# Kernel optimization log

Hardware: AMD Instinct MI355X
Metric: run time of the kernel (lower is better)

Reference implementation:

```python
import jax, jax.numpy as jnp
import numpy as np

B, D, E = 8192, 4096, 64
TOP_K = 2
NOISE_EPSILON = 0.01


def setup_inputs() -> dict:
    key = jax.random.key(0)
    k1, k2, k3, k4 = jax.random.split(key, 4)
    return {
        "x": jax.random.normal(k1, (B, D), dtype=jnp.float32),
        # nn.Linear weights, init std=0.1, no bias; torch stores [out, in]
        "gate_w": jax.random.normal(k2, (E, D), dtype=jnp.float32) * 0.1,
        "noise_gate_w": jax.random.normal(k3, (E, D), dtype=jnp.float32) * 0.1,
        # deterministic stand-in for torch.randn_like(clean_logits)
        "noise": jax.random.normal(k4, (B, E), dtype=jnp.float32),
    }


def reference(x, gate_w, noise_gate_w, noise):
    # clean_logits = x @ W_g^T : [B, E]
    clean_logits = jnp.einsum("bd,ed->be", x, gate_w)
    # training path: noisy logits with softplus-scaled noise
    noise_logits = jnp.einsum("bd,ed->be", x, noise_gate_w)
    noisy_logits = clean_logits + noise * jax.nn.softplus(noise_logits) * NOISE_EPSILON
    # top-k over experts, softmax over the k selected logits
    top_k_logits, top_k_indices = jax.lax.top_k(noisy_logits, TOP_K)  # [B, k]
    top_k_gates = jax.nn.softmax(top_k_logits, axis=-1)
    # scatter back into dense [B, E] gates
    rows = jnp.arange(noisy_logits.shape[0])[:, None]  # [B, 1]
    gates = jnp.zeros_like(noisy_logits).at[rows, top_k_indices].set(top_k_gates)
    load = jax.nn.softmax(clean_logits, axis=-1)
    return (gates, load)
```

## Files before the change

### kernel.cpp

```cpp
#include <hip/hip_runtime.h>
#include <math.h>

#define BB 8192
#define DD 4096
#define EE 64

constexpr float NOISE_EPS = 0.01f;
constexpr int BM  = 64;
constexpr int BK  = 32;

typedef __attribute__((ext_vector_type(8))) _Float16 f16x8;
typedef __attribute__((ext_vector_type(4))) float    f32x4;

__device__ __forceinline__ void split8(const float4& a, const float4& b,
                                       f16x8& hi, f16x8& mi) {
    float v[8] = {a.x, a.y, a.z, a.w, b.x, b.y, b.z, b.w};
    #pragma unroll
    for (int j = 0; j < 8; ++j) {
        _Float16 h = (_Float16)v[j];
        hi[j] = h;
        mi[j] = (_Float16)(v[j] - (float)h);
    }
}

__device__ __forceinline__ void gl_lds16(const void* g, void* l) {
    __builtin_amdgcn_global_load_lds(
        (const __attribute__((address_space(1))) unsigned*)g,
        (__attribute__((address_space(3))) unsigned*)l, 16, 0, 0);
}

__global__ __launch_bounds__(256) void wsplit_pack(
    const float* __restrict__ gw, const float* __restrict__ ngw,
    char* __restrict__ wpk)
{
    const int gid = blockIdx.x * 256 + threadIdx.x;
    const int r   = gid >> 9;
    const int kc  = gid & 511;
    const int k0  = kc * 8;
    const float* src = (r < EE) ? gw + (size_t)r * DD + k0
                                : ngw + (size_t)(r - EE) * DD + k0;
    float4 a = *reinterpret_cast<const float4*>(src);
    float4 b = *reinterpret_cast<const float4*>(src + 4);
    f16x8 hi, mi;
    split8(a, b, hi, mi);
    const int T    = k0 >> 5;
    const int kq   = (k0 >> 3) & 3;
    const int cb   = r >> 4;
    const int lane = kq * 16 + (r & 15);
    char* base = wpk + (size_t)T * 16384;
    *reinterpret_cast<f16x8*>(base + ((cb * 2 + 0) * 64 + lane) * 16) = hi;
    *reinterpret_cast<f16x8*>(base + ((cb * 2 + 1) * 64 + lane) * 16) = mi;
}

template <int SK>
__global__ __launch_bounds__(512, 4) void gating_main(
    const float* __restrict__ x,
    const char*  __restrict__ wpk,
    float* __restrict__ partial)
{
    constexpr int KC  = DD / SK;
    constexpr int NKS = KC / BK;

    __shared__ __align__(1024) char xbuf[3][8192];
    __shared__ __align__(1024) char wbuf[2][16384];

    const int tid  = threadIdx.x;
    const int bid  = blockIdx.x;
    const int sk   = bid & (SK - 1);
    const int row0 = (bid / SK) * BM;
    const int lane = tid & 63;
    const int wv   = tid >> 6;
    const int wmi  = wv >> 1;
    const int wni  = wv & 1;
    const int l15  = lane & 15;
    const int kq   = lane >> 4;

    const int xrow = tid >> 3;
    const int xch  = tid & 7;
    const float* xg = x + (size_t)(row0 + xrow) * DD + sk * KC
                        + ((xch ^ (xrow & 7)) << 2);
    const char* wg = wpk + (size_t)(sk * NKS) * 16384 + tid * 16;

    const int ldst = wv * 1024;

    const int ar = wmi * 16 + l15;
    const int xoff0 = ar * 128 + (((kq * 2 + 0) ^ (ar & 7)) << 4);
    const int xoff1 = ar * 128 + (((kq * 2 + 1) ^ (ar & 7)) << 4);
    int boff[4][2];
    #pragma unroll
    for (int nb = 0; nb < 4; ++nb) {
        const int cb = wni * 4 + nb;
        boff[nb][0] = ((cb * 2 + 0) * 64 + lane) * 16;
        boff[nb][1] = ((cb * 2 + 1) * 64 + lane) * 16;
    }

    f32x4 acc[4];
    #pragma unroll
    for (int nb = 0; nb < 4; ++nb) acc[nb] = {0.f, 0.f, 0.f, 0.f};

    char* xc  = (char*)xbuf[0];
    char* xn1 = (char*)xbuf[1];
    char* xn2 = (char*)xbuf[2];
    char* wc  = (char*)wbuf[0];
    char* wn  = (char*)wbuf[1];

    gl_lds16(wg,                wc + ldst);
    gl_lds16(wg + 8192,         wc + 8192 + ldst);
    gl_lds16(xg,                xc + ldst);
    gl_lds16(wg + 16384,        wn + ldst);
    gl_lds16(wg + 16384 + 8192, wn + 8192 + ldst);
    gl_lds16(xg + BK,           xn1 + ldst);
    gl_lds16(xg + 2 * BK,       xn2 + ldst);
    asm volatile("s_waitcnt vmcnt(4)" ::: "memory");
    __builtin_amdgcn_s_barrier();

    for (int t = 0; t < NKS; ++t) {
        f16x8 ah, am;
        {
            float4 a0 = *reinterpret_cast<const float4*>(xc + xoff0);
            float4 a1 = *reinterpret_cast<const float4*>(xc + xoff1);
            split8(a0, a1, ah, am);
        }
        #pragma unroll
        for (int nb = 0; nb < 4; ++nb) {
            f16x8 bh = *reinterpret_cast<const f16x8*>(wc + boff[nb][0]);
            f16x8 bm = *reinterpret_cast<const f16x8*>(wc + boff[nb][1]);
            acc[nb] = __builtin_amdgcn_mfma_f32_16x16x32_f16(ah, bh, acc[nb], 0, 0, 0);
            acc[nb] = __builtin_amdgcn_mfma_f32_16x16x32_f16(am, bh, acc[nb], 0, 0, 0);
            acc[nb] = __builtin_amdgcn_mfma_f32_16x16x32_f16(ah, bm, acc[nb], 0, 0, 0);
        }

        asm volatile("s_waitcnt lgkmcnt(0)" ::: "memory");
        __builtin_amdgcn_s_barrier();

        const int tw = (t + 2 < NKS) ? (t + 2) : (NKS - 1);
        const int tx = (t + 3 < NKS) ? (t + 3) : (NKS - 1);
        gl_lds16(wg + (size_t)tw * 16384,        wc + ldst);
        gl_lds16(wg + (size_t)tw * 16384 + 8192, wc + 8192 + ldst);
        gl_lds16(xg + (size_t)tx * BK,           xc + ldst);
        asm volatile("s_waitcnt vmcnt(4)" ::: "memory");
        __builtin_amdgcn_s_barrier();

        char* xt = xc; xc = xn1; xn1 = xn2; xn2 = xt;
        char* wt = wc; wc = wn;  wn  = wt;
    }
    asm volatile("s_waitcnt vmcnt(0)" ::: "memory");

    const size_t pbase = ((size_t)sk * BB + row0) * 128;
    #pragma unroll
    for (int nb = 0; nb < 4; ++nb) {
        #pragma unroll
        for (int j = 0; j < 4; ++j) {
            const int r = wmi * 16 + kq * 4 + j;
            const int c = wni * 64 + nb * 16 + l15;
            partial[pbase + (size_t)r * 128 + c] = acc[nb][j];
        }
    }
}

template <int SK>
__global__ __launch_bounds__(512) void gating_epi(
    const float* __restrict__ partial,
    const float* __restrict__ noise,
    float* __restrict__ out)
{
    const int tid  = threadIdx.x;
    const int wv   = tid >> 6;
    const int lane = tid & 63;
    const int l15  = lane & 15;
    const int kq   = lane >> 4;
    const int grow = blockIdx.x * 32 + wv * 4 + kq;
    const int s    = l15;

    const float* pb = partial + (size_t)grow * 128 + 4 * s;
    float4 c4 = {0.f,0.f,0.f,0.f}, n4 = {0.f,0.f,0.f,0.f};
    #pragma unroll
    for (int k = 0; k < SK; ++k) {
        const float* p = pb + (size_t)k * BB * 128;
        float4 a = *reinterpret_cast<const float4*>(p);
        float4 b = *reinterpret_cast<const float4*>(p + 64);
        c4.x += a.x; c4.y += a.y; c4.z += a.z; c4.w += a.w;
        n4.x += b.x; n4.y += b.y; n4.z += b.z; n4.w += b.w;
    }

    float4 nz = *reinterpret_cast<const float4*>(noise + (size_t)grow * EE + 4 * s);

    float cc[4] = {c4.x, c4.y, c4.z, c4.w};
    float nl[4] = {n4.x, n4.y, n4.z, n4.w};
    float m1 = -3.4e38f, m2 = -3.4e38f;
    int   i1 = -1, i2 = -1;
    float cmax = -3.4e38f;
    #pragma unroll
    for (int j = 0; j < 4; ++j) {
        const int e = 4 * s + j;
        float sp  = fmaxf(nl[j], 0.0f) + log1pf(expf(-fabsf(nl[j])));
        float nzj = (j == 0) ? nz.x : (j == 1) ? nz.y : (j == 2) ? nz.z : nz.w;
        float vno = fmaf(nzj * sp, NOISE_EPS, cc[j]);
        if (vno > m1)      { m2 = m1; i2 = i1; m1 = vno; i1 = e; }
        else if (vno > m2) { m2 = vno; i2 = e; }
        cmax = fmaxf(cmax, cc[j]);
    }

    #pragma unroll
    for (int m = 1; m < 16; m <<= 1) {
        float b1 = __shfl_xor(m1, m, 16);
        int  bi1 = __shfl_xor(i1, m, 16);
        float b2 = __shfl_xor(m2, m, 16);
        int  bi2 = __shfl_xor(i2, m, 16);
        cmax = fmaxf(cmax, __shfl_xor(cmax, m, 16));

        bool bwin = (b1 > m1) || (b1 == m1 && bi1 < i1);
        float t1; int ti1; float t2; int ti2;
        if (bwin) {
            t1 = b1; ti1 = bi1;
            bool aw = (m1 > b2) || (m1 == b2 && i1 < bi2);
            t2 = aw ? m1 : b2; ti2 = aw ? i1 : bi2;
        } else {
            t1 = m1; ti1 = i1;
            bool bw = (b1 > m2) || (b1 == m2 && bi1 < i2);
            t2 = bw ? b1 : m2; ti2 = bw ? bi1 : i2;
        }
        m1 = t1; i1 = ti1; m2 = t2; i2 = ti2;
    }

    float tq = expf(m2 - m1);
    float p1 = 1.0f / (1.0f + tq);
    float p2 = tq * p1;

    float e0 = expf(cc[0] - cmax);
    float e1 = expf(cc[1] - cmax);
    float e2 = expf(cc[2] - cmax);
    float e3 = expf(cc[3] - cmax);
    float sum = e0 + e1 + e2 + e3;
    #pragma unroll
    for (int m = 1; m < 16; m <<= 1) sum += __shfl_xor(sum, m, 16);
    float inv = 1.0f / sum;

    const int eb = 4 * s;
    float4 gt;
    gt.x = (eb     == i1) ? p1 : (eb     == i2) ? p2 : 0.0f;
    gt.y = (eb + 1 == i1) ? p1 : (eb + 1 == i2) ? p2 : 0.0f;
    gt.z = (eb + 2 == i1) ? p1 : (eb + 2 == i2) ? p2 : 0.0f;
    gt.w = (eb + 3 == i1) ? p1 : (eb + 3 == i2) ? p2 : 0.0f;
    float4 ld = {e0 * inv, e1 * inv, e2 * inv, e3 * inv};

    *reinterpret_cast<float4*>(out + (size_t)grow * EE + eb) = gt;
    *reinterpret_cast<float4*>(out + (size_t)BB * EE + (size_t)grow * EE + eb) = ld;
}

extern "C" void kernel_launch(void* const* d_in, const int* in_sizes, int n_in,
                              void* d_out, int out_size, void* d_ws, size_t ws_size,
                              hipStream_t stream) {
    const float* x     = (const float*)d_in[0];
    const float* gw    = (const float*)d_in[1];
    const float* ngw   = (const float*)d_in[2];
    const float* noise = (const float*)d_in[3];
    float* out = (float*)d_out;

    char*  wpk     = (char*)d_ws;
    float* partial = (float*)(wpk + (size_t)2 * 1024 * 1024);

    const size_t MB = 1024 * 1024;

    hipLaunchKernelGGL(wsplit_pack, dim3(256), dim3(256), 0, stream, gw, ngw, wpk);

    if (ws_size >= 18 * MB) {
        hipLaunchKernelGGL(gating_main<4>, dim3((BB / BM) * 4), dim3(512), 0, stream,
                           x, wpk, partial);
        hipLaunchKernelGGL(gating_epi<4>, dim3(BB / 32), dim3(512), 0, stream,
                           partial, noise, out);
    } else if (ws_size >= 10 * MB) {
        hipLaunchKernelGGL(gating_main<2>, dim3((BB / BM) * 2), dim3(512), 0, stream,
                           x, wpk, partial);
        hipLaunchKernelGGL(gating_epi<2>, dim3(BB / 32), dim3(512), 0, stream,
                           partial, noise, out);
    } else {
        hipLaunchKernelGGL(gating_main<1>, dim3(BB / BM), dim3(512), 0, stream,
                           x, wpk, partial);
        hipLaunchKernelGGL(gating_epi<1>, dim3(BB / 32), dim3(512), 0, stream,
                           partial, noise, out);
    }
}
```

Before: 52.17 us.

## Load packed weights directly to registers and retile waves as 2x4 grid

The weight tiles are no longer staged through LDS. Each wave loads its B fragments straight from global memory into registers, double-buffered one k-step ahead. Waves are rearranged into a 2x4 grid so each wave covers 32 rows and 32 columns, reusing its A fragments across two column blocks. The x ring grows to four buffers, and the loop is unrolled by two with a single barrier per step. This removes LDS traffic and a barrier for the weights but leans on L2 to serve duplicated weight loads, and it uses more registers.

```diff
diff --git a/kernel.cpp b/kernel.cpp
--- a/kernel.cpp
+++ b/kernel.cpp
@@ -61,8 +61,7 @@
     constexpr int KC  = DD / SK;
     constexpr int NKS = KC / BK;
 
-    __shared__ __align__(1024) char xbuf[3][8192];
-    __shared__ __align__(1024) char wbuf[2][16384];
+    __shared__ __align__(1024) char xbuf[4][8192];
 
     const int tid  = threadIdx.x;
     const int bid  = blockIdx.x;
@@ -70,8 +69,8 @@
     const int row0 = (bid / SK) * BM;
     const int lane = tid & 63;
     const int wv   = tid >> 6;
-    const int wmi  = wv >> 1;
-    const int wni  = wv & 1;
+    const int m2   = wv & 1;
+    const int n2   = wv >> 1;
     const int l15  = lane & 15;
     const int kq   = lane >> 4;
 
@@ -79,82 +78,102 @@
     const int xch  = tid & 7;
     const float* xg = x + (size_t)(row0 + xrow) * DD + sk * KC
                         + ((xch ^ (xrow & 7)) << 2);
-    const char* wg = wpk + (size_t)(sk * NKS) * 16384 + tid * 16;
-
     const int ldst = wv * 1024;
-
-    const int ar = wmi * 16 + l15;
-    const int xoff0 = ar * 128 + (((kq * 2 + 0) ^ (ar & 7)) << 4);
-    const int xoff1 = ar * 128 + (((kq * 2 + 1) ^ (ar & 7)) << 4);
-    int boff[4][2];
-    #pragma unroll
-    for (int nb = 0; nb < 4; ++nb) {
-        const int cb = wni * 4 + nb;
-        boff[nb][0] = ((cb * 2 + 0) * 64 + lane) * 16;
-        boff[nb][1] = ((cb * 2 + 1) * 64 + lane) * 16;
-    }
-
-    f32x4 acc[4];
-    #pragma unroll
-    for (int nb = 0; nb < 4; ++nb) acc[nb] = {0.f, 0.f, 0.f, 0.f};
-
-    char* xc  = (char*)xbuf[0];
-    char* xn1 = (char*)xbuf[1];
-    char* xn2 = (char*)xbuf[2];
-    char* wc  = (char*)wbuf[0];
-    char* wn  = (char*)wbuf[1];
-
-    gl_lds16(wg,                wc + ldst);
-    gl_lds16(wg + 8192,         wc + 8192 + ldst);
-    gl_lds16(xg,                xc + ldst);
-    gl_lds16(wg + 16384,        wn + ldst);
-    gl_lds16(wg + 16384 + 8192, wn + 8192 + ldst);
-    gl_lds16(xg + BK,           xn1 + ldst);
-    gl_lds16(xg + 2 * BK,       xn2 + ldst);
-    asm volatile("s_waitcnt vmcnt(4)" ::: "memory");
+    char* xls = (char*)&xbuf[0][0];
+
+    int xoff[2][2];
+    #pragma unroll
+    for (int mb = 0; mb < 2; ++mb) {
+        const int ar = m2 * 32 + mb * 16 + l15;
+        #pragma unroll
+        for (int u = 0; u < 2; ++u)
+            xoff[mb][u] = ar * 128 + (((kq * 2 + u) ^ (ar & 7)) << 4);
+    }
+
+    const char* wgB = wpk + ((size_t)(sk * NKS) << 14) + lane * 16;
+    const int off_h0 = ((n2 * 2 + 0) * 2 + 0) * 1024;
+    const int off_m0 = ((n2 * 2 + 0) * 2 + 1) * 1024;
+    const int off_h1 = ((n2 * 2 + 1) * 2 + 0) * 1024;
+    const int off_m1 = ((n2 * 2 + 1) * 2 + 1) * 1024;
+
+    f32x4 acc00 = {0.f,0.f,0.f,0.f}, acc01 = {0.f,0.f,0.f,0.f};
+    f32x4 acc10 = {0.f,0.f,0.f,0.f}, acc11 = {0.f,0.f,0.f,0.f};
+
+    #define LOADB(t, BH0, BM0, BH1, BM1) do {                                  \
+        const char* _b = wgB + ((size_t)(t) << 14);                            \
+        BH0 = *reinterpret_cast<const f16x8*>(_b + off_h0);                    \
+        BM0 = *reinterpret_cast<const f16x8*>(_b + off_m0);                    \
+        BH1 = *reinterpret_cast<const f16x8*>(_b + off_h1);                    \
+        BM1 = *reinterpret_cast<const f16x8*>(_b + off_m1);                    \
+    } while (0)
+
+    #define COMPUTE(t, BH0, BM0, BH1, BM1) do {                                \
+        const char* _xb = xls + (((t) & 3) << 13);                             \
+        float4 a00 = *reinterpret_cast<const float4*>(_xb + xoff[0][0]);       \
+        float4 a01 = *reinterpret_cast<const float4*>(_xb + xoff[0][1]);       \
+        float4 a10 = *reinterpret_cast<const float4*>(_xb + xoff[1][0]);       \
+        float4 a11 = *reinterpret_cast<const float4*>(_xb + xoff[1][1]);       \
+        f16x8 ah0, am0, ah1, am1;                                              \
+        split8(a00, a01, ah0, am0);                                            \
+        split8(a10, a11, ah1, am1);                                            \
+        acc00 = __builtin_amdgcn_mfma_f32_16x16x32_f16(ah0, BH0, acc00, 0,0,0);\
+        acc01 = __builtin_amdgcn_mfma_f32_16x16x32_f16(ah0, BH1, acc01, 0,0,0);\
+        acc10 = __builtin_amdgcn_mfma_f32_16x16x32_f16(ah1, BH0, acc10, 0,0,0);\
+        acc11 = __builtin_amdgcn_mfma_f32_16x16x32_f16(ah1, BH1, acc11, 0,0,0);\
+        acc00 = __builtin_amdgcn_mfma_f32_16x16x32_f16(am0, BH0, acc00, 0,0,0);\
+        acc01 = __builtin_amdgcn_mfma_f32_16x16x32_f16(am0, BH1, acc01, 0,0,0);\
+        acc10 = __builtin_amdgcn_mfma_f32_16x16x32_f16(am1, BH0, acc10, 0,0,0);\
+        acc11 = __builtin_amdgcn_mfma_f32_16x16x32_f16(am1, BH1, acc11, 0,0,0);\
+        acc00 = __builtin_amdgcn_mfma_f32_16x16x32_f16(ah0, BM0, acc00, 0,0,0);\
+        acc01 = __builtin_amdgcn_mfma_f32_16x16x32_f16(ah0, BM1, acc01, 0,0,0);\
+        acc10 = __builtin_amdgcn_mfma_f32_16x16x32_f16(ah1, BM0, acc10, 0,0,0);\
+        acc11 = __builtin_amdgcn_mfma_f32_16x16x32_f16(ah1, BM1, acc11, 0,0,0);\
+    } while (0)
+
+    f16x8 pH0, pM0, pH1, pM1;
+    f16x8 qH0, qM0, qH1, qM1;
+
+    gl_lds16(xg,            xls + ldst);
+    gl_lds16(xg + BK,       xls + 8192 + ldst);
+    gl_lds16(xg + 2 * BK,   xls + 16384 + ldst);
+    LOADB(0, pH0, pM0, pH1, pM1);
+    asm volatile("s_waitcnt vmcnt(0)" ::: "memory");
     __builtin_amdgcn_s_barrier();
 
-    for (int t = 0; t < NKS; ++t) {
-        f16x8 ah, am;
+    for (int t = 0; t < NKS; t += 2) {
         {
-            float4 a0 = *reinterpret_cast<const float4*>(xc + xoff0);
-            float4 a1 = *reinterpret_cast<const float4*>(xc + xoff1);
-            split8(a0, a1, ah, am);
+            const int tb = (t + 1 < NKS) ? t + 1 : NKS - 1;
+            LOADB(tb, qH0, qM0, qH1, qM1);
+            asm volatile("s_waitcnt vmcnt(5)" ::: "memory");
+            __builtin_amdgcn_s_barrier();
+            const int tx = (t + 3 < NKS) ? t + 3 : NKS - 1;
+            gl_lds16(xg + (size_t)tx * BK, xls + (((t + 3) & 3) << 13) + ldst);
+            COMPUTE(t, pH0, pM0, pH1, pM1);
         }
-        #pragma unroll
-        for (int nb = 0; nb < 4; ++nb) {
-            f16x8 bh = *reinterpret_cast<const f16x8*>(wc + boff[nb][0]);
-            f16x8 bm = *reinterpret_cast<const f16x8*>(wc + boff[nb][1]);
-            acc[nb] = __builtin_amdgcn_mfma_f32_16x16x32_f16(ah, bh, acc[nb], 0, 0, 0);
-            acc[nb] = __builtin_amdgcn_mfma_f32_16x16x32_f16(am, bh, acc[nb], 0, 0, 0);
-            acc[nb] = __builtin_amdgcn_mfma_f32_16x16x32_f16(ah, bm, acc[nb], 0, 0, 0);
+        {
+            const int tb = (t + 2 < NKS) ? t + 2 : NKS - 1;
+            LOADB(tb, pH0, pM0, pH1, pM1);
+            asm volatile("s_waitcnt vmcnt(5)" ::: "memory");
+            __builtin_amdgcn_s_barrier();
+            const int tx = (t + 4 < NKS) ? t + 4 : NKS - 1;
+            gl_lds16(xg + (size_t)tx * BK, xls + (((t + 4) & 3) << 13) + ldst);
+            COMPUTE(t + 1, qH0, qM0, qH1, qM1);
         }
-
-        asm volatile("s_waitcnt lgkmcnt(0)" ::: "memory");
-        __builtin_amdgcn_s_barrier();
-
-        const int tw = (t + 2 < NKS) ? (t + 2) : (NKS - 1);
-        const int tx = (t + 3 < NKS) ? (t + 3) : (NKS - 1);
-        gl_lds16(wg + (size_t)tw * 16384,        wc + ldst);
-        gl_lds16(wg + (size_t)tw * 16384 + 8192, wc + 8192 + ldst);
-        gl_lds16(xg + (size_t)tx * BK,           xc + ldst);
-        asm volatile("s_waitcnt vmcnt(4)" ::: "memory");
-        __builtin_amdgcn_s_barrier();
-
-        char* xt = xc; xc = xn1; xn1 = xn2; xn2 = xt;
-        char* wt = wc; wc = wn;  wn  = wt;
     }
     asm volatile("s_waitcnt vmcnt(0)" ::: "memory");
 
+    #undef LOADB
+    #undef COMPUTE
+
     const size_t pbase = ((size_t)sk * BB + row0) * 128;
     #pragma unroll
-    for (int nb = 0; nb < 4; ++nb) {
-        #pragma unroll
-        for (int j = 0; j < 4; ++j) {
-            const int r = wmi * 16 + kq * 4 + j;
-            const int c = wni * 64 + nb * 16 + l15;
-            partial[pbase + (size_t)r * 128 + c] = acc[nb][j];
-        }
+    for (int j = 0; j < 4; ++j) {
+        const int r0 = m2 * 32 + kq * 4 + j;
+        const int c0 = n2 * 32 + l15;
+        partial[pbase + (size_t)r0 * 128 + c0]             = acc00[j];
+        partial[pbase + (size_t)r0 * 128 + c0 + 16]        = acc01[j];
+        partial[pbase + (size_t)(r0 + 16) * 128 + c0]      = acc10[j];
+        partial[pbase + (size_t)(r0 + 16) * 128 + c0 + 16] = acc11[j];
     }
 }
 
```

Result: slower. 55.20 us (+5.8%).

## Split x once into LDS and stream pre-split weights directly to registers

Applied to the files above, without the earlier changes.

The main GEMM loop is restructured. Each x tile is loaded through registers, split once into fp16 hi/mid parts, and written to swizzled LDS, so the split is no longer redone per wave. Each wave now owns one 16-column expert block across all 64 rows, and reads its packed weight fragments straight from global memory into registers two chunks ahead, with no LDS staging. The direct-to-LDS async loads and triple buffering are replaced by a double-buffered LDS scheme over a 64-wide K step. This risks exposed global latency on the weight loads and higher register pressure.

```diff
diff --git a/kernel.cpp b/kernel.cpp
--- a/kernel.cpp
+++ b/kernel.cpp
@@ -6,8 +6,7 @@
 #define EE 64
 
 constexpr float NOISE_EPS = 0.01f;
-constexpr int BM  = 64;
-constexpr int BK  = 32;
+constexpr int BM = 64;
 
 typedef __attribute__((ext_vector_type(8))) _Float16 f16x8;
 typedef __attribute__((ext_vector_type(4))) float    f32x4;
@@ -21,12 +20,6 @@
         hi[j] = h;
         mi[j] = (_Float16)(v[j] - (float)h);
     }
-}
-
-__device__ __forceinline__ void gl_lds16(const void* g, void* l) {
-    __builtin_amdgcn_global_load_lds(
-        (const __attribute__((address_space(1))) unsigned*)g,
-        (__attribute__((address_space(3))) unsigned*)l, 16, 0, 0);
 }
 
 __global__ __launch_bounds__(256) void wsplit_pack(
@@ -58,102 +51,139 @@
     const char*  __restrict__ wpk,
     float* __restrict__ partial)
 {
-    constexpr int KC  = DD / SK;
-    constexpr int NKS = KC / BK;
-
-    __shared__ __align__(1024) char xbuf[3][8192];
-    __shared__ __align__(1024) char wbuf[2][16384];
+    constexpr int KC   = DD / SK;
+    constexpr int NKS  = KC / 64;
+    constexpr int GMAX = 2 * NKS - 1;
+
+    __shared__ __align__(1024) char xls[2][16384];
 
     const int tid  = threadIdx.x;
     const int bid  = blockIdx.x;
     const int sk   = bid & (SK - 1);
     const int row0 = (bid / SK) * BM;
     const int lane = tid & 63;
-    const int wv   = tid >> 6;
-    const int wmi  = wv >> 1;
-    const int wni  = wv & 1;
+    const int n8   = tid >> 6;
     const int l15  = lane & 15;
     const int kq   = lane >> 4;
 
-    const int xrow = tid >> 3;
-    const int xch  = tid & 7;
-    const float* xg = x + (size_t)(row0 + xrow) * DD + sk * KC
-                        + ((xch ^ (xrow & 7)) << 2);
-    const char* wg = wpk + (size_t)(sk * NKS) * 16384 + tid * 16;
-
-    const int ldst = wv * 1024;
-
-    const int ar = wmi * 16 + l15;
-    const int xoff0 = ar * 128 + (((kq * 2 + 0) ^ (ar & 7)) << 4);
-    const int xoff1 = ar * 128 + (((kq * 2 + 1) ^ (ar & 7)) << 4);
-    int boff[4][2];
-    #pragma unroll
-    for (int nb = 0; nb < 4; ++nb) {
-        const int cb = wni * 4 + nb;
-        boff[nb][0] = ((cb * 2 + 0) * 64 + lane) * 16;
-        boff[nb][1] = ((cb * 2 + 1) * 64 + lane) * 16;
-    }
-
-    f32x4 acc[4];
-    #pragma unroll
-    for (int nb = 0; nb < 4; ++nb) acc[nb] = {0.f, 0.f, 0.f, 0.f};
-
-    char* xc  = (char*)xbuf[0];
-    char* xn1 = (char*)xbuf[1];
-    char* xn2 = (char*)xbuf[2];
-    char* wc  = (char*)wbuf[0];
-    char* wn  = (char*)wbuf[1];
-
-    gl_lds16(wg,                wc + ldst);
-    gl_lds16(wg + 8192,         wc + 8192 + ldst);
-    gl_lds16(xg,                xc + ldst);
-    gl_lds16(wg + 16384,        wn + ldst);
-    gl_lds16(wg + 16384 + 8192, wn + 8192 + ldst);
-    gl_lds16(xg + BK,           xn1 + ldst);
-    gl_lds16(xg + 2 * BK,       xn2 + ldst);
-    asm volatile("s_waitcnt vmcnt(4)" ::: "memory");
-    __builtin_amdgcn_s_barrier();
-
-    for (int t = 0; t < NKS; ++t) {
-        f16x8 ah, am;
-        {
-            float4 a0 = *reinterpret_cast<const float4*>(xc + xoff0);
-            float4 a1 = *reinterpret_cast<const float4*>(xc + xoff1);
-            split8(a0, a1, ah, am);
-        }
-        #pragma unroll
-        for (int nb = 0; nb < 4; ++nb) {
-            f16x8 bh = *reinterpret_cast<const f16x8*>(wc + boff[nb][0]);
-            f16x8 bm = *reinterpret_cast<const f16x8*>(wc + boff[nb][1]);
-            acc[nb] = __builtin_amdgcn_mfma_f32_16x16x32_f16(ah, bh, acc[nb], 0, 0, 0);
-            acc[nb] = __builtin_amdgcn_mfma_f32_16x16x32_f16(am, bh, acc[nb], 0, 0, 0);
-            acc[nb] = __builtin_amdgcn_mfma_f32_16x16x32_f16(ah, bm, acc[nb], 0, 0, 0);
-        }
-
+    const int sr = tid >> 3;
+    const int sj = tid & 7;
+    const float* xg = x + (size_t)(row0 + sr) * DD + sk * KC + sj * 8;
+    const int wo0 = sr * 256 + 0 * 128 + ((sj ^ (sr & 7)) << 4);
+    const int wo1 = sr * 256 + 1 * 128 + ((sj ^ (sr & 7)) << 4);
+
+    int rbase[4], swz[4];
+    #pragma unroll
+    for (int ms = 0; ms < 4; ++ms) {
+        const int r = ms * 16 + l15;
+        rbase[ms] = r * 256;
+        swz[ms]   = r & 7;
+    }
+
+    const char* wpkB = wpk + ((size_t)(sk * NKS * 2) << 14) + lane * 16;
+    const int oh = (2 * n8 + 0) * 1024;
+    const int om = (2 * n8 + 1) * 1024;
+
+    f32x4 acc0 = {0.f,0.f,0.f,0.f}, acc1 = {0.f,0.f,0.f,0.f};
+    f32x4 acc2 = {0.f,0.f,0.f,0.f}, acc3 = {0.f,0.f,0.f,0.f};
+
+    #define LOADB(g, H, M) do {                                                \
+        const char* _b = wpkB + ((size_t)(g) << 14);                           \
+        H = *reinterpret_cast<const f16x8*>(_b + oh);                          \
+        M = *reinterpret_cast<const f16x8*>(_b + om);                          \
+    } while (0)
+
+    #define CHUNK(bufp, gc, H, M) do {                                         \
+        const char* _xb = (bufp);                                              \
+        const int _c = (gc) & 1;                                               \
+        f16x8 ah0 = *reinterpret_cast<const f16x8*>(_xb + rbase[0] +           \
+                        ((((_c << 2) | kq) ^ swz[0]) << 4));                   \
+        f16x8 am0 = *reinterpret_cast<const f16x8*>(_xb + rbase[0] + 128 +     \
+                        ((((_c << 2) | kq) ^ swz[0]) << 4));                   \
+        f16x8 ah1 = *reinterpret_cast<const f16x8*>(_xb + rbase[1] +           \
+                        ((((_c << 2) | kq) ^ swz[1]) << 4));                   \
+        f16x8 am1 = *reinterpret_cast<const f16x8*>(_xb + rbase[1] + 128 +     \
+                        ((((_c << 2) | kq) ^ swz[1]) << 4));                   \
+        f16x8 ah2 = *reinterpret_cast<const f16x8*>(_xb + rbase[2] +           \
+                        ((((_c << 2) | kq) ^ swz[2]) << 4));                   \
+        f16x8 am2 = *reinterpret_cast<const f16x8*>(_xb + rbase[2] + 128 +     \
+                        ((((_c << 2) | kq) ^ swz[2]) << 4));                   \
+        f16x8 ah3 = *reinterpret_cast<const f16x8*>(_xb + rbase[3] +           \
+                        ((((_c << 2) | kq) ^ swz[3]) << 4));                   \
+        f16x8 am3 = *reinterpret_cast<const f16x8*>(_xb + rbase[3] + 128 +     \
+                        ((((_c << 2) | kq) ^ swz[3]) << 4));                   \
+        acc0 = __builtin_amdgcn_mfma_f32_16x16x32_f16(ah0, H, acc0, 0,0,0);    \
+        acc1 = __builtin_amdgcn_mfma_f32_16x16x32_f16(ah1, H, acc1, 0,0,0);    \
+        acc2 = __builtin_amdgcn_mfma_f32_16x16x32_f16(ah2, H, acc2, 0,0,0);    \
+        acc3 = __builtin_amdgcn_mfma_f32_16x16x32_f16(ah3, H, acc3, 0,0,0);    \
+        acc0 = __builtin_amdgcn_mfma_f32_16x16x32_f16(am0, H, acc0, 0,0,0);    \
+        acc1 = __builtin_amdgcn_mfma_f32_16x16x32_f16(am1, H, acc1, 0,0,0);    \
+        acc2 = __builtin_amdgcn_mfma_f32_16x16x32_f16(am2, H, acc2, 0,0,0);    \
+        acc3 = __builtin_amdgcn_mfma_f32_16x16x32_f16(am3, H, acc3, 0,0,0);    \
+        acc0 = __builtin_amdgcn_mfma_f32_16x16x32_f16(ah0, M, acc0, 0,0,0);    \
+        acc1 = __builtin_amdgcn_mfma_f32_16x16x32_f16(ah1, M, acc1, 0,0,0);    \
+        acc2 = __builtin_amdgcn_mfma_f32_16x16x32_f16(ah2, M, acc2, 0,0,0);    \
+        acc3 = __builtin_amdgcn_mfma_f32_16x16x32_f16(ah3, M, acc3, 0,0,0);    \
+        { const int _g = (gc) + 2;                                             \
+          LOADB((_g <= GMAX) ? _g : GMAX, H, M); }                             \
+    } while (0)
+
+    #define WSPLIT(bp, V0, V1) do {                                            \
+        f16x8 _hi, _mi;                                                        \
+        split8(V0, V1, _hi, _mi);                                              \
+        *reinterpret_cast<f16x8*>((bp) + wo0) = _hi;                           \
+        *reinterpret_cast<f16x8*>((bp) + wo1) = _mi;                           \
+    } while (0)
+
+    char* buf0 = (char*)xls[0];
+    char* buf1 = (char*)xls[1];
+
+    float4 xA0, xA1, xB0, xB1;
+    f16x8 pH, pM, qH, qM;
+
+    xA0 = *reinterpret_cast<const float4*>(xg);
+    xA1 = *reinterpret_cast<const float4*>(xg + 4);
+    xB0 = *reinterpret_cast<const float4*>(xg + 64);
+    xB1 = *reinterpret_cast<const float4*>(xg + 64 + 4);
+    WSPLIT(buf0, xA0, xA1);
+    LOADB(0, pH, pM);
+    LOADB(1, qH, qM);
+
+    for (int t = 0; t < NKS; t += 2) {
         asm volatile("s_waitcnt lgkmcnt(0)" ::: "memory");
         __builtin_amdgcn_s_barrier();
-
-        const int tw = (t + 2 < NKS) ? (t + 2) : (NKS - 1);
-        const int tx = (t + 3 < NKS) ? (t + 3) : (NKS - 1);
-        gl_lds16(wg + (size_t)tw * 16384,        wc + ldst);
-        gl_lds16(wg + (size_t)tw * 16384 + 8192, wc + 8192 + ldst);
-        gl_lds16(xg + (size_t)tx * BK,           xc + ldst);
-        asm volatile("s_waitcnt vmcnt(4)" ::: "memory");
+        if (t + 2 < NKS) {
+            xA0 = *reinterpret_cast<const float4*>(xg + (size_t)(t + 2) * 64);
+            xA1 = *reinterpret_cast<const float4*>(xg + (size_t)(t + 2) * 64 + 4);
+        }
+        WSPLIT(buf1, xB0, xB1);
+        CHUNK(buf0, 2 * t,     pH, pM);
+        CHUNK(buf0, 2 * t + 1, qH, qM);
+
+        asm volatile("s_waitcnt lgkmcnt(0)" ::: "memory");
         __builtin_amdgcn_s_barrier();
-
-        char* xt = xc; xc = xn1; xn1 = xn2; xn2 = xt;
-        char* wt = wc; wc = wn;  wn  = wt;
-    }
-    asm volatile("s_waitcnt vmcnt(0)" ::: "memory");
+        if (t + 3 < NKS) {
+            xB0 = *reinterpret_cast<const float4*>(xg + (size_t)(t + 3) * 64);
+            xB1 = *reinterpret_cast<const float4*>(xg + (size_t)(t + 3) * 64 + 4);
+        }
+        if (t + 2 < NKS) WSPLIT(buf0, xA0, xA1);
+        CHUNK(buf1, 2 * t + 2, pH, pM);
+        CHUNK(buf1, 2 * t + 3, qH, qM);
+    }
+
+    #undef LOADB
+    #undef CHUNK
+    #undef WSPLIT
 
     const size_t pbase = ((size_t)sk * BB + row0) * 128;
     #pragma unroll
-    for (int nb = 0; nb < 4; ++nb) {
+    for (int ms = 0; ms < 4; ++ms) {
+        f32x4 a = (ms == 0) ? acc0 : (ms == 1) ? acc1 : (ms == 2) ? acc2 : acc3;
         #pragma unroll
         for (int j = 0; j < 4; ++j) {
-            const int r = wmi * 16 + kq * 4 + j;
-            const int c = wni * 64 + nb * 16 + l15;
-            partial[pbase + (size_t)r * 128 + c] = acc[nb][j];
+            const int r = ms * 16 + kq * 4 + j;
+            const int c = n8 * 16 + l15;
+            partial[pbase + (size_t)r * 128 + c] = a[j];
         }
     }
 }
```

Measured after the change: 49.69 us. 1.05x faster.

## Pre-split x into LDS once per tile and stream weights via registers

Applied to the files above, without the earlier changes.

Restructures the gating GEMM. Rows are split into hi/lo f16 once per 256-wide K stage and stored in double-buffered, swizzled LDS, where the old kernel re-split x in every MFMA-feeding thread. Each wave now owns 16 output columns, and its weight fragments are prefetched straight from global memory into registers two steps ahead, so they no longer pass through LDS. The row tile shrinks to 32 and split-K drops from 4 to 2, which changes the grid shape and the partial-buffer size. The risks are more register pressure from the prefetched weight fragments and fewer barriers hiding global latency.

```diff
diff --git a/kernel.cpp b/kernel.cpp
--- a/kernel.cpp
+++ b/kernel.cpp
@@ -6,8 +6,7 @@
 #define EE 64
 
 constexpr float NOISE_EPS = 0.01f;
-constexpr int BM  = 64;
-constexpr int BK  = 32;
+constexpr int BM = 32;
 
 typedef __attribute__((ext_vector_type(8))) _Float16 f16x8;
 typedef __attribute__((ext_vector_type(4))) float    f32x4;
@@ -21,12 +20,6 @@
         hi[j] = h;
         mi[j] = (_Float16)(v[j] - (float)h);
     }
-}
-
-__device__ __forceinline__ void gl_lds16(const void* g, void* l) {
-    __builtin_amdgcn_global_load_lds(
-        (const __attribute__((address_space(1))) unsigned*)g,
-        (__attribute__((address_space(3))) unsigned*)l, 16, 0, 0);
 }
 
 __global__ __launch_bounds__(256) void wsplit_pack(
@@ -58,11 +51,11 @@
     const char*  __restrict__ wpk,
     float* __restrict__ partial)
 {
-    constexpr int KC  = DD / SK;
-    constexpr int NKS = KC / BK;
-
-    __shared__ __align__(1024) char xbuf[3][8192];
-    __shared__ __align__(1024) char wbuf[2][16384];
+    constexpr int KC   = DD / SK;
+    constexpr int NMS  = KC / 256;
+    constexpr int GMAX = KC / 32 - 1;
+
+    __shared__ __align__(1024) char xls[2][32768];
 
     const int tid  = threadIdx.x;
     const int bid  = blockIdx.x;
@@ -70,91 +63,108 @@
     const int row0 = (bid / SK) * BM;
     const int lane = tid & 63;
     const int wv   = tid >> 6;
-    const int wmi  = wv >> 1;
-    const int wni  = wv & 1;
     const int l15  = lane & 15;
     const int kq   = lane >> 4;
 
-    const int xrow = tid >> 3;
-    const int xch  = tid & 7;
-    const float* xg = x + (size_t)(row0 + xrow) * DD + sk * KC
-                        + ((xch ^ (xrow & 7)) << 2);
-    const char* wg = wpk + (size_t)(sk * NKS) * 16384 + tid * 16;
-
-    const int ldst = wv * 1024;
-
-    const int ar = wmi * 16 + l15;
-    const int xoff0 = ar * 128 + (((kq * 2 + 0) ^ (ar & 7)) << 4);
-    const int xoff1 = ar * 128 + (((kq * 2 + 1) ^ (ar & 7)) << 4);
-    int boff[4][2];
-    #pragma unroll
-    for (int nb = 0; nb < 4; ++nb) {
-        const int cb = wni * 4 + nb;
-        boff[nb][0] = ((cb * 2 + 0) * 64 + lane) * 16;
-        boff[nb][1] = ((cb * 2 + 1) * 64 + lane) * 16;
-    }
-
-    f32x4 acc[4];
-    #pragma unroll
-    for (int nb = 0; nb < 4; ++nb) acc[nb] = {0.f, 0.f, 0.f, 0.f};
-
-    char* xc  = (char*)xbuf[0];
-    char* xn1 = (char*)xbuf[1];
-    char* xn2 = (char*)xbuf[2];
-    char* wc  = (char*)wbuf[0];
-    char* wn  = (char*)wbuf[1];
-
-    gl_lds16(wg,                wc + ldst);
-    gl_lds16(wg + 8192,         wc + 8192 + ldst);
-    gl_lds16(xg,                xc + ldst);
-    gl_lds16(wg + 16384,        wn + ldst);
-    gl_lds16(wg + 16384 + 8192, wn + 8192 + ldst);
-    gl_lds16(xg + BK,           xn1 + ldst);
-    gl_lds16(xg + 2 * BK,       xn2 + ldst);
-    asm volatile("s_waitcnt vmcnt(4)" ::: "memory");
-    __builtin_amdgcn_s_barrier();
-
-    for (int t = 0; t < NKS; ++t) {
-        f16x8 ah, am;
-        {
-            float4 a0 = *reinterpret_cast<const float4*>(xc + xoff0);
-            float4 a1 = *reinterpret_cast<const float4*>(xc + xoff1);
-            split8(a0, a1, ah, am);
-        }
-        #pragma unroll
-        for (int nb = 0; nb < 4; ++nb) {
-            f16x8 bh = *reinterpret_cast<const f16x8*>(wc + boff[nb][0]);
-            f16x8 bm = *reinterpret_cast<const f16x8*>(wc + boff[nb][1]);
-            acc[nb] = __builtin_amdgcn_mfma_f32_16x16x32_f16(ah, bh, acc[nb], 0, 0, 0);
-            acc[nb] = __builtin_amdgcn_mfma_f32_16x16x32_f16(am, bh, acc[nb], 0, 0, 0);
-            acc[nb] = __builtin_amdgcn_mfma_f32_16x16x32_f16(ah, bm, acc[nb], 0, 0, 0);
-        }
-
+    const int sr = tid >> 4;
+    const int ss = tid & 15;
+    const float* xg = x + (size_t)(row0 + sr) * DD + sk * KC + ss * 16;
+    const int swr = sr & 7;
+    const int wo_h0 = sr * 1024 +       (((2 * ss)     ^ swr) << 4);
+    const int wo_h1 = sr * 1024 +       (((2 * ss + 1) ^ swr) << 4);
+    const int wo_m0 = sr * 1024 + 512 + (((2 * ss)     ^ swr) << 4);
+    const int wo_m1 = sr * 1024 + 512 + (((2 * ss + 1) ^ swr) << 4);
+
+    const int rb0 = (l15) * 1024,      swz0 = l15 & 7;
+    const int rb1 = (16 + l15) * 1024, swz1 = (16 + l15) & 7;
+
+    const char* wpkB = wpk + ((size_t)(sk * (KC / 32)) << 14)
+                           + wv * 2048 + lane * 16;
+
+    f32x4 acc0 = {0.f, 0.f, 0.f, 0.f};
+    f32x4 acc1 = {0.f, 0.f, 0.f, 0.f};
+
+    #define LOADB(g, H, M) do {                                                \
+        const char* _b = wpkB + ((size_t)(g) << 14);                           \
+        H = *reinterpret_cast<const f16x8*>(_b);                               \
+        M = *reinterpret_cast<const f16x8*>(_b + 1024);                        \
+    } while (0)
+
+    #define LOADX(t) do {                                                      \
+        const float* _s = xg + (size_t)(t) * 256;                              \
+        xa0 = *reinterpret_cast<const float4*>(_s);                            \
+        xa1 = *reinterpret_cast<const float4*>(_s + 4);                        \
+        xa2 = *reinterpret_cast<const float4*>(_s + 8);                        \
+        xa3 = *reinterpret_cast<const float4*>(_s + 12);                       \
+    } while (0)
+
+    #define WSPLIT(bp) do {                                                    \
+        f16x8 _h, _m;                                                          \
+        split8(xa0, xa1, _h, _m);                                              \
+        *reinterpret_cast<f16x8*>((bp) + wo_h0) = _h;                          \
+        *reinterpret_cast<f16x8*>((bp) + wo_m0) = _m;                          \
+        split8(xa2, xa3, _h, _m);                                              \
+        *reinterpret_cast<f16x8*>((bp) + wo_h1) = _h;                          \
+        *reinterpret_cast<f16x8*>((bp) + wo_m1) = _m;                          \
+    } while (0)
+
+    #define CHUNK(c, H, M) do {                                                \
+        const int _s0 = (((c) * 4 + kq) ^ swz0) << 4;                          \
+        const int _s1 = (((c) * 4 + kq) ^ swz1) << 4;                          \
+        f16x8 ah0 = *reinterpret_cast<const f16x8*>(bufc + rb0 + _s0);         \
+        f16x8 am0 = *reinterpret_cast<const f16x8*>(bufc + rb0 + 512 + _s0);   \
+        f16x8 ah1 = *reinterpret_cast<const f16x8*>(bufc + rb1 + _s1);         \
+        f16x8 am1 = *reinterpret_cast<const f16x8*>(bufc + rb1 + 512 + _s1);   \
+        acc0 = __builtin_amdgcn_mfma_f32_16x16x32_f16(ah0, H, acc0, 0, 0, 0);  \
+        acc1 = __builtin_amdgcn_mfma_f32_16x16x32_f16(ah1, H, acc1, 0, 0, 0);  \
+        acc0 = __builtin_amdgcn_mfma_f32_16x16x32_f16(am0, H, acc0, 0, 0, 0);  \
+        acc1 = __builtin_amdgcn_mfma_f32_16x16x32_f16(am1, H, acc1, 0, 0, 0);  \
+        acc0 = __builtin_amdgcn_mfma_f32_16x16x32_f16(ah0, M, acc0, 0, 0, 0);  \
+        acc1 = __builtin_amdgcn_mfma_f32_16x16x32_f16(ah1, M, acc1, 0, 0, 0);  \
+        { const int _g = gbase + (c) + 2;                                      \
+          LOADB((_g <= GMAX) ? _g : GMAX, H, M); }                             \
+    } while (0)
+
+    float4 xa0, xa1, xa2, xa3;
+    f16x8 pH, pM, qH, qM;
+
+    LOADX(0);
+    WSPLIT(xls[0]);
+    LOADB(0, pH, pM);
+    LOADB(1, qH, qM);
+
+    for (int t = 0; t < NMS; ++t) {
         asm volatile("s_waitcnt lgkmcnt(0)" ::: "memory");
         __builtin_amdgcn_s_barrier();
 
-        const int tw = (t + 2 < NKS) ? (t + 2) : (NKS - 1);
-        const int tx = (t + 3 < NKS) ? (t + 3) : (NKS - 1);
-        gl_lds16(wg + (size_t)tw * 16384,        wc + ldst);
-        gl_lds16(wg + (size_t)tw * 16384 + 8192, wc + 8192 + ldst);
-        gl_lds16(xg + (size_t)tx * BK,           xc + ldst);
-        asm volatile("s_waitcnt vmcnt(4)" ::: "memory");
-        __builtin_amdgcn_s_barrier();
-
-        char* xt = xc; xc = xn1; xn1 = xn2; xn2 = xt;
-        char* wt = wc; wc = wn;  wn  = wt;
-    }
-    asm volatile("s_waitcnt vmcnt(0)" ::: "memory");
+        if (t + 1 < NMS) LOADX(t + 1);
+
+        const char* bufc = xls[t & 1];
+        const int gbase = t * 8;
+        CHUNK(0, pH, pM);
+        CHUNK(1, qH, qM);
+        CHUNK(2, pH, pM);
+        CHUNK(3, qH, qM);
+        CHUNK(4, pH, pM);
+        CHUNK(5, qH, qM);
+        CHUNK(6, pH, pM);
+        CHUNK(7, qH, qM);
+
+        if (t + 1 < NMS) WSPLIT(xls[(t + 1) & 1]);
+    }
+
+    #undef LOADB
+    #undef LOADX
+    #undef WSPLIT
+    #undef CHUNK
 
     const size_t pbase = ((size_t)sk * BB + row0) * 128;
     #pragma unroll
-    for (int nb = 0; nb < 4; ++nb) {
-        #pragma unroll
-        for (int j = 0; j < 4; ++j) {
-            const int r = wmi * 16 + kq * 4 + j;
-            const int c = wni * 64 + nb * 16 + l15;
-            partial[pbase + (size_t)r * 128 + c] = acc[nb][j];
-        }
+    for (int j = 0; j < 4; ++j) {
+        const int r0 = kq * 4 + j;
+        const int c  = wv * 16 + l15;
+        partial[pbase + (size_t)r0 * 128 + c]        = acc0[j];
+        partial[pbase + (size_t)(r0 + 16) * 128 + c] = acc1[j];
     }
 }
 
@@ -264,12 +274,7 @@
 
     hipLaunchKernelGGL(wsplit_pack, dim3(256), dim3(256), 0, stream, gw, ngw, wpk);
 
-    if (ws_size >= 18 * MB) {
-        hipLaunchKernelGGL(gating_main<4>, dim3((BB / BM) * 4), dim3(512), 0, stream,
-                           x, wpk, partial);
-        hipLaunchKernelGGL(gating_epi<4>, dim3(BB / 32), dim3(512), 0, stream,
-                           partial, noise, out);
-    } else if (ws_size >= 10 * MB) {
+    if (ws_size >= 11 * MB) {
         hipLaunchKernelGGL(gating_main<2>, dim3((BB / BM) * 2), dim3(512), 0, stream,
                            x, wpk, partial);
         hipLaunchKernelGGL(gating_epi<2>, dim3(BB / 32), dim3(512), 0, stream,
```

Result: slower. 60.24 us (+15.5%).
